# Kernel optimization log

Measured on AMD Instinct MI355X. Metric: run time of the kernel, lower is better.

## Reference

```python
import jax, jax.numpy as jnp
import numpy as np

B, M, N, D, NH, DH = 2, 2048, 2048, 1024, 16, 64
STD = 0.02

def setup_inputs() -> dict:
    key = jax.random.key(0)
    ks = jax.random.split(key, 7)
    query = jax.random.normal(ks[0], (B, M, D), dtype=jnp.float32)
    key_value = jax.random.normal(ks[1], (B, N, D), dtype=jnp.float32)
    key_padding_mask = jax.random.uniform(ks[2], (B, N)) < 0.1
    # torch Linear weight is (out,in); store as (in,out) for x @ W
    W_Q = STD * jax.random.truncated_normal(ks[3], -2.0, 2.0, (D, NH * DH), dtype=jnp.float32)
    W_K = STD * jax.random.truncated_normal(ks[4], -2.0, 2.0, (D, NH * DH), dtype=jnp.float32)
    W_V = STD * jax.random.truncated_normal(ks[5], -2.0, 2.0, (D, NH * DH), dtype=jnp.float32)
    W_O = STD * jax.random.truncated_normal(ks[6], -2.0, 2.0, (NH * DH, D), dtype=jnp.float32)
    return {"query": query, "key_value": key_value, "key_padding_mask": key_padding_mask,
            "W_Q": W_Q, "W_K": W_K, "W_V": W_V, "W_O": W_O}

def reference(query, key_value, key_padding_mask, W_Q, W_K, W_V, W_O):
    scale = 1.0 / jnp.sqrt(jnp.float32(DH))
    Q = (query @ W_Q).reshape(B, M, NH, DH)       # (B,M,H,dh)
    K = (key_value @ W_K).reshape(B, N, NH, DH)   # (B,N,H,dh)
    V = (key_value @ W_V).reshape(B, N, NH, DH)
    scores = jnp.einsum('bmhd,bnhd->bhmn', Q, K) * scale  # (B,H,M,N)
    scores = jnp.where(key_padding_mask[:, None, None, :], -jnp.inf, scores)
    attn = jax.nn.softmax(scores, axis=-1)
    out = jnp.einsum('bhmn,bnhd->bmhd', attn, V).reshape(B, M, NH * DH)
    return out @ W_O
```

## Files before the change

### kernel.cpp

```cpp
#include <hip/hip_runtime.h>
#include <math.h>

#define BB 2
#define SEQ 2048
#define DMODEL 1024
#define NHH 16
#define DHH 64

typedef __bf16 bf16;
typedef __attribute__((ext_vector_type(8))) __bf16 bf16x8;
typedef __attribute__((ext_vector_type(4))) float f32x4;
typedef __attribute__((ext_vector_type(16))) float f32x16;

#define C1f 0.18033688011112042f
#define C2f -5.770780163555854f

__device__ __forceinline__ uint32_t cvtpk_bf16(float lo, float hi) {
  uint32_t r;
  asm("v_cvt_pk_bf16_f32 %0, %1, %2" : "=v"(r) : "v"(lo), "v"(hi));
  return r;
}
__device__ __forceinline__ void pl32swap(uint32_t& a, uint32_t& b) {
  asm("v_permlane32_swap_b32 %0, %1" : "+v"(a), "+v"(b));
}

__device__ __forceinline__ void gl_lds16(const bf16* g, bf16* l) {
  __builtin_amdgcn_global_load_lds(
      (const __attribute__((address_space(1))) void*)g,
      (__attribute__((address_space(3))) void*)l, 16, 0, 0);
}

__global__ __launch_bounds__(256) void prep(const float* __restrict__ query,
                                            const float* __restrict__ key_value,
                                            bf16* __restrict__ qbf,
                                            bf16* __restrict__ kvbf,
                                            const float* __restrict__ W0, const float* __restrict__ W1,
                                            const float* __restrict__ W2, const float* __restrict__ W3,
                                            bf16* __restrict__ O0, bf16* __restrict__ O1,
                                            bf16* __restrict__ O2, bf16* __restrict__ O3) {
  __shared__ bf16 T[64][72];
  const int bid = blockIdx.x;
  const int t = threadIdx.x;
  if (bid >= 1024) {
    const int bidc = bid - 1024;
    const float* in = (bidc >> 11) ? key_value : query;
    bf16* out = (bidc >> 11) ? kvbf : qbf;
    const int i = (bidc & 2047) * 256 + t;
    const float4* p = (const float4*)in + 2 * (size_t)i;
    float4 a = p[0], b = p[1];
    bf16x8 v;
    v[0] = (bf16)a.x; v[1] = (bf16)a.y; v[2] = (bf16)a.z; v[3] = (bf16)a.w;
    v[4] = (bf16)b.x; v[5] = (bf16)b.y; v[6] = (bf16)b.z; v[7] = (bf16)b.w;
    *((bf16x8*)out + i) = v;
    return;
  }
  const float* W; bf16* O;
  switch (bid >> 8) {
    case 0: W = W0; O = O0; break;
    case 1: W = W1; O = O1; break;
    case 2: W = W2; O = O2; break;
    default: W = W3; O = O3; break;
  }
  const int n0 = (bid & 15) * 64, k0 = ((bid >> 4) & 15) * 64;
  {
    int k = t >> 2, ns = (t & 3) * 16;
    const float* g = W + (size_t)(k0 + k) * DMODEL + n0 + ns;
#pragma unroll
    for (int q = 0; q < 4; ++q) {
      float4 f = *(const float4*)(g + 4 * q);
      T[ns + 4 * q + 0][k] = (bf16)f.x;
      T[ns + 4 * q + 1][k] = (bf16)f.y;
      T[ns + 4 * q + 2][k] = (bf16)f.z;
      T[ns + 4 * q + 3][k] = (bf16)f.w;
    }
  }
  __syncthreads();
  {
    int n = t >> 2, ks = (t & 3) * 16;
    bf16x8 a = *(const bf16x8*)&T[n][ks];
    bf16x8 b = *(const bf16x8*)&T[n][ks + 8];
    bf16* o = O + (size_t)(n0 + n) * DMODEL + k0 + ks;
    *(bf16x8*)o = a;
    *(bf16x8*)(o + 8) = b;
  }
}

template <bool F32OUT>
__device__ __forceinline__ void gemm128_body(const bf16* __restrict__ A,
                                             const bf16* __restrict__ Bt,
                                             float* __restrict__ Cf,
                                             bf16* __restrict__ Cb,
                                             bf16* As0, bf16* Bs0,
                                             bf16* As1, bf16* Bs1) {
  const int t = threadIdx.x;
  const int lane = t & 63, wave = t >> 6;
  const int l15 = lane & 15, quad = lane >> 4;
  const int bm = blockIdx.y * 128, bn = blockIdx.x * 128;
  const int wr = wave >> 1, wc = wave & 1;

  const int srow = wave * 32 + (lane >> 3);
  const int sc = lane & 7;
  const int ca = sc ^ ((lane >> 3) & 7);
  const bf16* gA = A + (size_t)(bm + srow) * DMODEL + ca * 8;
  const bf16* gB = Bt + (size_t)(bn + srow) * DMODEL + ca * 8;
  const int lo = wave * 32 * 64;

  f32x4 acc[4][4] = {};

#define STAGE(KT, AS, BS)                                                \
  {                                                                      \
    const int kk = (KT) * 64;                                            \
    _Pragma("unroll") for (int j = 0; j < 4; ++j) {                      \
      gl_lds16(gA + (size_t)(j * 8) * DMODEL + kk, (AS) + lo + j * 512); \
      gl_lds16(gB + (size_t)(j * 8) * DMODEL + kk, (BS) + lo + j * 512); \
    }                                                                    \
  }

#define COMPUTE(AS, BS)                                                \
  {                                                                    \
    _Pragma("unroll") for (int ks = 0; ks < 2; ++ks) {                 \
      bf16x8 af[4], bfr[4];                                            \
      _Pragma("unroll") for (int mt = 0; mt < 4; ++mt) {               \
        int row = wr * 64 + mt * 16 + l15;                             \
        int s = (ks * 4 + quad) ^ (row & 7);                           \
        af[mt] = *(const bf16x8*)&(AS)[row * 64 + s * 8];              \
      }                                                                \
      _Pragma("unroll") for (int nt = 0; nt < 4; ++nt) {               \
        int row = wc * 64 + nt * 16 + l15;                             \
        int s = (ks * 4 + quad) ^ (row & 7);                           \
        bfr[nt] = *(const bf16x8*)&(BS)[row * 64 + s * 8];             \
      }                                                                \
      _Pragma("unroll") for (int mt = 0; mt < 4; ++mt)                 \
          _Pragma("unroll") for (int nt = 0; nt < 4; ++nt)             \
              acc[mt][nt] = __builtin_amdgcn_mfma_f32_16x16x32_bf16(   \
                  af[mt], bfr[nt], acc[mt][nt], 0, 0, 0);              \
    }                                                                  \
  }

  STAGE(0, As0, Bs0);
  __syncthreads();

  for (int kt = 0; kt < DMODEL / 64; kt += 2) {
    if (kt + 1 < DMODEL / 64) STAGE(kt + 1, As1, Bs1);
    COMPUTE(As0, Bs0);
    __syncthreads();
    if (kt + 2 < DMODEL / 64) STAGE(kt + 2, As0, Bs0);
    COMPUTE(As1, Bs1);
    __syncthreads();
  }
#undef STAGE
#undef COMPUTE

#pragma unroll
  for (int mt = 0; mt < 4; ++mt)
#pragma unroll
    for (int nt = 0; nt < 4; ++nt)
#pragma unroll
      for (int r = 0; r < 4; ++r) {
        int row = bm + wr * 64 + mt * 16 + quad * 4 + r;
        int col = bn + wc * 64 + nt * 16 + l15;
        if (F32OUT) Cf[(size_t)row * DMODEL + col] = acc[mt][nt][r];
        else Cb[(size_t)row * DMODEL + col] = (bf16)acc[mt][nt][r];
      }
}

__global__ __launch_bounds__(256, 2) void gemm_qkv(const bf16* __restrict__ qbf,
                                                   const bf16* __restrict__ kvbf,
                                                   const bf16* __restrict__ WtQ,
                                                   const bf16* __restrict__ WtK,
                                                   const bf16* __restrict__ WtV,
                                                   bf16* __restrict__ Qb,
                                                   bf16* __restrict__ Kb,
                                                   bf16* __restrict__ Vb) {
  __shared__ bf16 As0[128 * 64], Bs0[128 * 64];
  __shared__ bf16 As1[128 * 64], Bs1[128 * 64];
  const bf16 *A, *Bt; bf16* C;
  switch (blockIdx.z) {
    case 0: A = qbf; Bt = WtQ; C = Qb; break;
    case 1: A = kvbf; Bt = WtK; C = Kb; break;
    default: A = kvbf; Bt = WtV; C = Vb; break;
  }
  gemm128_body<false>(A, Bt, nullptr, C, As0, Bs0, As1, Bs1);
}

__global__ __launch_bounds__(256, 2) void gemm_out(const bf16* __restrict__ A,
                                                   const bf16* __restrict__ Wt,
                                                   float* __restrict__ C) {
  __shared__ bf16 As0[128 * 64], Bs0[128 * 64];
  __shared__ bf16 As1[128 * 64], Bs1[128 * 64];
  gemm128_body<true>(A, Wt, C, nullptr, As0, Bs0, As1, Bs1);
}

__global__ __launch_bounds__(256) void attn_mfma(const bf16* __restrict__ Qb,
                                                 const bf16* __restrict__ Kb,
                                                 const bf16* __restrict__ Vb,
                                                 const int* __restrict__ maskp,
                                                 bf16* __restrict__ Ob) {
  __shared__ bf16 Ks[2][64 * 64];
  __shared__ bf16 Vt[2][64][68];

  const int blk = blockIdx.x;
  const int h = blk & 15;
  const int b = (blk >> 4) & 1;
  const int qb = blk >> 5;
  const int t = threadIdx.x;
  const int wave = t >> 6, lane = t & 63;
  const int l31 = lane & 31, hi = lane >> 5;

  const int kr = t >> 2, kq = t & 3;
  const bf16* gK = Kb + (size_t)(b * SEQ + kr) * DMODEL + h * 64 + kq * 16;
  const int s0 = (kq * 2) ^ (kr & 7), s1 = (kq * 2 + 1) ^ (kr & 7);
  const int nv = (t & 31) * 2, dc = (t >> 5) * 8;
  const bf16* gV = Vb + (size_t)(b * SEQ + nv) * DMODEL + h * 64 + dc;
  const int* gM = maskp + b * SEQ;

  {
    bf16x8 k0 = *(const bf16x8*)(gK);
    bf16x8 k1 = *(const bf16x8*)(gK + 8);
    *(bf16x8*)&Ks[0][kr * 64 + s0 * 8] = k0;
    *(bf16x8*)&Ks[0][kr * 64 + s1 * 8] = k1;
    bf16x8 v0 = *(const bf16x8*)(gV);
    bf16x8 v1 = *(const bf16x8*)(gV + DMODEL);
    union U { bf16x8 v; uint32_t dw[4]; } a, c;
    a.v = v0; c.v = v1;
#pragma unroll
    for (int d2 = 0; d2 < 4; ++d2) {
      *(uint32_t*)&Vt[0][dc + 2 * d2 + 0][nv] = __builtin_amdgcn_perm(c.dw[d2], a.dw[d2], 0x05040100u);
      *(uint32_t*)&Vt[0][dc + 2 * d2 + 1][nv] = __builtin_amdgcn_perm(c.dw[d2], a.dw[d2], 0x07060302u);
    }
  }
  int mcur = gM[lane];

  bf16x8 qf[4];
#pragma unroll
  for (int ks = 0; ks < 4; ++ks) {
    const bf16* g = Qb + (size_t)(b * SEQ + qb * 128 + wave * 32 + l31) * DMODEL +
                    h * 64 + ks * 16 + hi * 8;
    qf[ks] = *(const bf16x8*)g;
  }

  f32x16 o0 = {}, o1 = {};
  float lsum = 0.f;

  __syncthreads();

  for (int it = 0; it < SEQ / 64; ++it) {
    const int p = it & 1;
    const bool more = (it + 1) < SEQ / 64;

    bf16x8 kreg0, kreg1, vreg0, vreg1;
    int mnext = 0;
    if (more) {
      const int nn = (it + 1) * 64;
      const bf16* gK2 = gK + (size_t)nn * DMODEL;
      const bf16* gV2 = gV + (size_t)nn * DMODEL;
      kreg0 = *(const bf16x8*)(gK2);
      kreg1 = *(const bf16x8*)(gK2 + 8);
      vreg0 = *(const bf16x8*)(gV2);
      vreg1 = *(const bf16x8*)(gV2 + DMODEL);
      mnext = gM[nn + lane];
    }

    f32x16 s0v = {}, s1v = {};
#pragma unroll
    for (int ks = 0; ks < 4; ++ks) {
      const int c = ks * 2 + hi;
      const int r0 = l31;
      const int r1 = 32 + l31;
      bf16x8 ka0 = *(const bf16x8*)&Ks[p][r0 * 64 + (c ^ (r0 & 7)) * 8];
      bf16x8 ka1 = *(const bf16x8*)&Ks[p][r1 * 64 + (c ^ (r1 & 7)) * 8];
      s0v = __builtin_amdgcn_mfma_f32_32x32x16_bf16(ka0, qf[ks], s0v, 0, 0, 0);
      s1v = __builtin_amdgcn_mfma_f32_32x32x16_bf16(ka1, qf[ks], s1v, 0, 0, 0);
    }

    const unsigned long long mb = __ballot(mcur == 0);

#pragma unroll
    for (int kt = 0; kt < 2; ++kt) {
      const f32x16 sv = kt ? s1v : s0v;
      const uint32_t ml = (uint32_t)(mb >> (kt * 32 + 4 * hi));
      float pm[16];
#pragma unroll
      for (int r = 0; r < 16; ++r) {
        const int bitc = (r & 3) + 8 * (r >> 2);
        float pex = __builtin_amdgcn_exp2f(sv[r] * C1f + C2f);
        pm[r] = ((ml >> bitc) & 1u) ? pex : 0.f;
        lsum += pm[r];
      }
      uint32_t w01 = cvtpk_bf16(pm[0], pm[1]),  w23 = cvtpk_bf16(pm[2], pm[3]);
      uint32_t w45 = cvtpk_bf16(pm[4], pm[5]),  w67 = cvtpk_bf16(pm[6], pm[7]);
      uint32_t w89 = cvtpk_bf16(pm[8], pm[9]),  wab = cvtpk_bf16(pm[10], pm[11]);
      uint32_t wcd = cvtpk_bf16(pm[12], pm[13]), wef = cvtpk_bf16(pm[14], pm[15]);
      pl32swap(w01, w45);
      pl32swap(w23, w67);
      pl32swap(w89, wcd);
      pl32swap(wab, wef);
      union BF { uint32_t u[4]; bf16x8 v; } f0, f1;
      f0.u[0] = w01; f0.u[1] = w23; f0.u[2] = w45; f0.u[3] = w67;
      f1.u[0] = w89; f1.u[1] = wab; f1.u[2] = wcd; f1.u[3] = wef;
      {
        bf16x8 va00 = *(const bf16x8*)&Vt[p][0 + l31][(kt * 2 + 0) * 16 + hi * 8];
        bf16x8 va01 = *(const bf16x8*)&Vt[p][0 + l31][(kt * 2 + 1) * 16 + hi * 8];
        o0 = __builtin_amdgcn_mfma_f32_32x32x16_bf16(va00, f0.v, o0, 0, 0, 0);
        o0 = __builtin_amdgcn_mfma_f32_32x32x16_bf16(va01, f1.v, o0, 0, 0, 0);
        bf16x8 va10 = *(const bf16x8*)&Vt[p][32 + l31][(kt * 2 + 0) * 16 + hi * 8];
        bf16x8 va11 = *(const bf16x8*)&Vt[p][32 + l31][(kt * 2 + 1) * 16 + hi * 8];
        o1 = __builtin_amdgcn_mfma_f32_32x32x16_bf16(va10, f0.v, o1, 0, 0, 0);
        o1 = __builtin_amdgcn_mfma_f32_32x32x16_bf16(va11, f1.v, o1, 0, 0, 0);
      }
    }

    if (more) {
      const int q = 1 - p;
      *(bf16x8*)&Ks[q][kr * 64 + s0 * 8] = kreg0;
      *(bf16x8*)&Ks[q][kr * 64 + s1 * 8] = kreg1;
      union U { bf16x8 v; uint32_t dw[4]; } a, c;
      a.v = vreg0; c.v = vreg1;
#pragma unroll
      for (int d2 = 0; d2 < 4; ++d2) {
        *(uint32_t*)&Vt[q][dc + 2 * d2 + 0][nv] = __builtin_amdgcn_perm(c.dw[d2], a.dw[d2], 0x05040100u);
        *(uint32_t*)&Vt[q][dc + 2 * d2 + 1][nv] = __builtin_amdgcn_perm(c.dw[d2], a.dw[d2], 0x07060302u);
      }
    }
    mcur = mnext;
    __syncthreads();
  }

  const float lt = lsum + __shfl_xor(lsum, 32);
  const float inv = 1.f / lt;
  bf16* gO = Ob + (size_t)(b * SEQ + qb * 128 + wave * 32 + l31) * DMODEL + h * 64;
#pragma unroll
  for (int g = 0; g < 4; ++g) {
    uint2 st0, st1;
    st0.x = cvtpk_bf16(o0[4 * g + 0] * inv, o0[4 * g + 1] * inv);
    st0.y = cvtpk_bf16(o0[4 * g + 2] * inv, o0[4 * g + 3] * inv);
    st1.x = cvtpk_bf16(o1[4 * g + 0] * inv, o1[4 * g + 1] * inv);
    st1.y = cvtpk_bf16(o1[4 * g + 2] * inv, o1[4 * g + 3] * inv);
    *(uint2*)(gO + 8 * g + 4 * hi) = st0;
    *(uint2*)(gO + 32 + 8 * g + 4 * hi) = st1;
  }
}

extern "C" void kernel_launch(void* const* d_in, const int* in_sizes, int n_in,
                              void* d_out, int out_size, void* d_ws, size_t ws_size,
                              hipStream_t stream) {
  (void)in_sizes; (void)n_in; (void)out_size; (void)ws_size;
  const float* query = (const float*)d_in[0];
  const float* key_value = (const float*)d_in[1];
  const int* mask = (const int*)d_in[2];
  const float* W_Q = (const float*)d_in[3];
  const float* W_K = (const float*)d_in[4];
  const float* W_V = (const float*)d_in[5];
  const float* W_O = (const float*)d_in[6];
  float* out = (float*)d_out;

  const size_t TOK = (size_t)BB * SEQ;
  const size_t TE = TOK * DMODEL;
  char* w = (char*)d_ws;
  bf16* qbf = (bf16*)w;   w += TE * 2;
  bf16* kvbf = (bf16*)w;  w += TE * 2;
  bf16* WtQ = (bf16*)w;   w += (size_t)DMODEL * DMODEL * 2;
  bf16* WtK = (bf16*)w;   w += (size_t)DMODEL * DMODEL * 2;
  bf16* WtV = (bf16*)w;   w += (size_t)DMODEL * DMODEL * 2;
  bf16* WtO = (bf16*)w;   w += (size_t)DMODEL * DMODEL * 2;
  bf16* Qbuf = (bf16*)w;  w += TE * 2;
  bf16* Kbuf = (bf16*)w;  w += TE * 2;
  bf16* Vbuf = (bf16*)w;  w += TE * 2;
  bf16* Obuf = (bf16*)w;  w += TE * 2;

  prep<<<5120, 256, 0, stream>>>(query, key_value, qbf, kvbf,
                                 W_Q, W_K, W_V, W_O, WtQ, WtK, WtV, WtO);

  gemm_qkv<<<dim3(DMODEL / 128, TOK / 128, 3), 256, 0, stream>>>(qbf, kvbf, WtQ, WtK, WtV,
                                                                 Qbuf, Kbuf, Vbuf);

  attn_mfma<<<BB * NHH * (SEQ / 128), 256, 0, stream>>>(Qbuf, Kbuf, Vbuf, mask, Obuf);

  gemm_out<<<dim3(DMODEL / 128, TOK / 128), 256, 0, stream>>>(Obuf, WtO, out);
}
```

Baseline: 212.5 us.

## Split key range across two wave groups per attention block and reduce partials

The attention block grows to 512 threads. Two groups of four waves each process half of the key/value sequence for the same 128 query rows, with separate double-buffered K/V shared tiles per group. At the end, the partial output accumulators and row sums are merged through shared memory reused from the K tile, and group 1 normalizes and writes the result. This doubles the resident waves per block to hide latency, at the cost of an extra LDS reduction. The K tile also drops its XOR swizzle in favour of padded rows, which may change bank-conflict behaviour.

```diff
diff --git a/kernel.cpp b/kernel.cpp
--- a/kernel.cpp
+++ b/kernel.cpp
@@ -191,13 +191,13 @@
   gemm128_body<true>(A, Wt, C, nullptr, As0, Bs0, As1, Bs1);
 }
 
-__global__ __launch_bounds__(256) void attn_mfma(const bf16* __restrict__ Qb,
-                                                 const bf16* __restrict__ Kb,
-                                                 const bf16* __restrict__ Vb,
-                                                 const int* __restrict__ maskp,
-                                                 bf16* __restrict__ Ob) {
-  __shared__ bf16 Ks[2][64 * 64];
-  __shared__ bf16 Vt[2][64][68];
+__global__ __launch_bounds__(512, 4) void attn_mfma(const bf16* __restrict__ Qb,
+                                                    const bf16* __restrict__ Kb,
+                                                    const bf16* __restrict__ Vb,
+                                                    const int* __restrict__ maskp,
+                                                    bf16* __restrict__ Ob) {
+  __shared__ bf16 Ks[2][2][64][68];
+  __shared__ bf16 Vt[2][2][64][68];
 
   const int blk = blockIdx.x;
   const int h = blk & 15;
@@ -205,28 +205,30 @@
   const int qb = blk >> 5;
   const int t = threadIdx.x;
   const int wave = t >> 6, lane = t & 63;
+  const int grp = wave >> 2;
+  const int w4 = wave & 3;
   const int l31 = lane & 31, hi = lane >> 5;
-
-  const int kr = t >> 2, kq = t & 3;
-  const bf16* gK = Kb + (size_t)(b * SEQ + kr) * DMODEL + h * 64 + kq * 16;
-  const int s0 = (kq * 2) ^ (kr & 7), s1 = (kq * 2 + 1) ^ (kr & 7);
-  const int nv = (t & 31) * 2, dc = (t >> 5) * 8;
-  const bf16* gV = Vb + (size_t)(b * SEQ + nv) * DMODEL + h * 64 + dc;
-  const int* gM = maskp + b * SEQ;
+  const int tl = t & 255;
+
+  const int kr = tl >> 2, kq = tl & 3;
+  const bf16* gK = Kb + (size_t)(b * SEQ + grp * 1024 + kr) * DMODEL + h * 64 + kq * 16;
+  const int nv = (tl & 31) * 2, dc = (tl >> 5) * 8;
+  const bf16* gV = Vb + (size_t)(b * SEQ + grp * 1024 + nv) * DMODEL + h * 64 + dc;
+  const int* gM = maskp + b * SEQ + grp * 1024;
 
   {
     bf16x8 k0 = *(const bf16x8*)(gK);
     bf16x8 k1 = *(const bf16x8*)(gK + 8);
-    *(bf16x8*)&Ks[0][kr * 64 + s0 * 8] = k0;
-    *(bf16x8*)&Ks[0][kr * 64 + s1 * 8] = k1;
+    *(bf16x8*)&Ks[grp][0][kr][kq * 16] = k0;
+    *(bf16x8*)&Ks[grp][0][kr][kq * 16 + 8] = k1;
     bf16x8 v0 = *(const bf16x8*)(gV);
     bf16x8 v1 = *(const bf16x8*)(gV + DMODEL);
     union U { bf16x8 v; uint32_t dw[4]; } a, c;
     a.v = v0; c.v = v1;
 #pragma unroll
     for (int d2 = 0; d2 < 4; ++d2) {
-      *(uint32_t*)&Vt[0][dc + 2 * d2 + 0][nv] = __builtin_amdgcn_perm(c.dw[d2], a.dw[d2], 0x05040100u);
-      *(uint32_t*)&Vt[0][dc + 2 * d2 + 1][nv] = __builtin_amdgcn_perm(c.dw[d2], a.dw[d2], 0x07060302u);
+      *(uint32_t*)&Vt[grp][0][dc + 2 * d2 + 0][nv] = __builtin_amdgcn_perm(c.dw[d2], a.dw[d2], 0x05040100u);
+      *(uint32_t*)&Vt[grp][0][dc + 2 * d2 + 1][nv] = __builtin_amdgcn_perm(c.dw[d2], a.dw[d2], 0x07060302u);
     }
   }
   int mcur = gM[lane];
@@ -234,7 +236,7 @@
   bf16x8 qf[4];
 #pragma unroll
   for (int ks = 0; ks < 4; ++ks) {
-    const bf16* g = Qb + (size_t)(b * SEQ + qb * 128 + wave * 32 + l31) * DMODEL +
+    const bf16* g = Qb + (size_t)(b * SEQ + qb * 128 + w4 * 32 + l31) * DMODEL +
                     h * 64 + ks * 16 + hi * 8;
     qf[ks] = *(const bf16x8*)g;
   }
@@ -244,9 +246,9 @@
 
   __syncthreads();
 
-  for (int it = 0; it < SEQ / 64; ++it) {
+  for (int it = 0; it < 16; ++it) {
     const int p = it & 1;
-    const bool more = (it + 1) < SEQ / 64;
+    const bool more = (it + 1) < 16;
 
     bf16x8 kreg0, kreg1, vreg0, vreg1;
     int mnext = 0;
@@ -264,11 +266,9 @@
     f32x16 s0v = {}, s1v = {};
 #pragma unroll
     for (int ks = 0; ks < 4; ++ks) {
-      const int c = ks * 2 + hi;
-      const int r0 = l31;
-      const int r1 = 32 + l31;
-      bf16x8 ka0 = *(const bf16x8*)&Ks[p][r0 * 64 + (c ^ (r0 & 7)) * 8];
-      bf16x8 ka1 = *(const bf16x8*)&Ks[p][r1 * 64 + (c ^ (r1 & 7)) * 8];
+      const int c = (ks * 2 + hi) * 8;
+      bf16x8 ka0 = *(const bf16x8*)&Ks[grp][p][l31][c];
+      bf16x8 ka1 = *(const bf16x8*)&Ks[grp][p][32 + l31][c];
       s0v = __builtin_amdgcn_mfma_f32_32x32x16_bf16(ka0, qf[ks], s0v, 0, 0, 0);
       s1v = __builtin_amdgcn_mfma_f32_32x32x16_bf16(ka1, qf[ks], s1v, 0, 0, 0);
     }
@@ -299,12 +299,12 @@
       f0.u[0] = w01; f0.u[1] = w23; f0.u[2] = w45; f0.u[3] = w67;
       f1.u[0] = w89; f1.u[1] = wab; f1.u[2] = wcd; f1.u[3] = wef;
       {
-        bf16x8 va00 = *(const bf16x8*)&Vt[p][0 + l31][(kt * 2 + 0) * 16 + hi * 8];
-        bf16x8 va01 = *(const bf16x8*)&Vt[p][0 + l31][(kt * 2 + 1) * 16 + hi * 8];
+        bf16x8 va00 = *(const bf16x8*)&Vt[grp][p][0 + l31][(kt * 2 + 0) * 16 + hi * 8];
+        bf16x8 va01 = *(const bf16x8*)&Vt[grp][p][0 + l31][(kt * 2 + 1) * 16 + hi * 8];
         o0 = __builtin_amdgcn_mfma_f32_32x32x16_bf16(va00, f0.v, o0, 0, 0, 0);
         o0 = __builtin_amdgcn_mfma_f32_32x32x16_bf16(va01, f1.v, o0, 0, 0, 0);
-        bf16x8 va10 = *(const bf16x8*)&Vt[p][32 + l31][(kt * 2 + 0) * 16 + hi * 8];
-        bf16x8 va11 = *(const bf16x8*)&Vt[p][32 + l31][(kt * 2 + 1) * 16 + hi * 8];
+        bf16x8 va10 = *(const bf16x8*)&Vt[grp][p][32 + l31][(kt * 2 + 0) * 16 + hi * 8];
+        bf16x8 va11 = *(const bf16x8*)&Vt[grp][p][32 + l31][(kt * 2 + 1) * 16 + hi * 8];
         o1 = __builtin_amdgcn_mfma_f32_32x32x16_bf16(va10, f0.v, o1, 0, 0, 0);
         o1 = __builtin_amdgcn_mfma_f32_32x32x16_bf16(va11, f1.v, o1, 0, 0, 0);
       }
@@ -312,32 +312,55 @@
 
     if (more) {
       const int q = 1 - p;
-      *(bf16x8*)&Ks[q][kr * 64 + s0 * 8] = kreg0;
-      *(bf16x8*)&Ks[q][kr * 64 + s1 * 8] = kreg1;
+      *(bf16x8*)&Ks[grp][q][kr][kq * 16] = kreg0;
+      *(bf16x8*)&Ks[grp][q][kr][kq * 16 + 8] = kreg1;
       union U { bf16x8 v; uint32_t dw[4]; } a, c;
       a.v = vreg0; c.v = vreg1;
 #pragma unroll
       for (int d2 = 0; d2 < 4; ++d2) {
-        *(uint32_t*)&Vt[q][dc + 2 * d2 + 0][nv] = __builtin_amdgcn_perm(c.dw[d2], a.dw[d2], 0x05040100u);
-        *(uint32_t*)&Vt[q][dc + 2 * d2 + 1][nv] = __builtin_amdgcn_perm(c.dw[d2], a.dw[d2], 0x07060302u);
+        *(uint32_t*)&Vt[grp][q][dc + 2 * d2 + 0][nv] = __builtin_amdgcn_perm(c.dw[d2], a.dw[d2], 0x05040100u);
+        *(uint32_t*)&Vt[grp][q][dc + 2 * d2 + 1][nv] = __builtin_amdgcn_perm(c.dw[d2], a.dw[d2], 0x07060302u);
       }
     }
     mcur = mnext;
     __syncthreads();
   }
 
-  const float lt = lsum + __shfl_xor(lsum, 32);
-  const float inv = 1.f / lt;
-  bf16* gO = Ob + (size_t)(b * SEQ + qb * 128 + wave * 32 + l31) * DMODEL + h * 64;
-#pragma unroll
-  for (int g = 0; g < 4; ++g) {
-    uint2 st0, st1;
-    st0.x = cvtpk_bf16(o0[4 * g + 0] * inv, o0[4 * g + 1] * inv);
-    st0.y = cvtpk_bf16(o0[4 * g + 2] * inv, o0[4 * g + 3] * inv);
-    st1.x = cvtpk_bf16(o1[4 * g + 0] * inv, o1[4 * g + 1] * inv);
-    st1.y = cvtpk_bf16(o1[4 * g + 2] * inv, o1[4 * g + 3] * inv);
-    *(uint2*)(gO + 8 * g + 4 * hi) = st0;
-    *(uint2*)(gO + 32 + 8 * g + 4 * hi) = st1;
+  const float ltp = lsum + __shfl_xor(lsum, 32);
+
+  float* sc = (float*)&Ks[0][0][0][0];
+  float* scO = sc + 256;
+
+  if (hi == 0) sc[wave * 32 + l31] = ltp;
+  if (grp == 0) {
+    float* dst = scO + ((size_t)(w4 * 64 + lane)) * 33;
+#pragma unroll
+    for (int r = 0; r < 16; ++r) {
+      dst[r] = o0[r];
+      dst[16 + r] = o1[r];
+    }
+  }
+  __syncthreads();
+  if (grp == 1) {
+    const float ltot = sc[w4 * 32 + l31] + sc[(4 + w4) * 32 + l31];
+    const float inv = 1.f / ltot;
+    const float* src = scO + ((size_t)(w4 * 64 + lane)) * 33;
+#pragma unroll
+    for (int r = 0; r < 16; ++r) {
+      o0[r] += src[r];
+      o1[r] += src[16 + r];
+    }
+    bf16* gO = Ob + (size_t)(b * SEQ + qb * 128 + w4 * 32 + l31) * DMODEL + h * 64;
+#pragma unroll
+    for (int g = 0; g < 4; ++g) {
+      uint2 st0, st1;
+      st0.x = cvtpk_bf16(o0[4 * g + 0] * inv, o0[4 * g + 1] * inv);
+      st0.y = cvtpk_bf16(o0[4 * g + 2] * inv, o0[4 * g + 3] * inv);
+      st1.x = cvtpk_bf16(o1[4 * g + 0] * inv, o1[4 * g + 1] * inv);
+      st1.y = cvtpk_bf16(o1[4 * g + 2] * inv, o1[4 * g + 3] * inv);
+      *(uint2*)(gO + 8 * g + 4 * hi) = st0;
+      *(uint2*)(gO + 32 + 8 * g + 4 * hi) = st1;
+    }
   }
 }
 
@@ -374,7 +397,7 @@
   gemm_qkv<<<dim3(DMODEL / 128, TOK / 128, 3), 256, 0, stream>>>(qbf, kvbf, WtQ, WtK, WtV,
                                                                  Qbuf, Kbuf, Vbuf);
 
-  attn_mfma<<<BB * NHH * (SEQ / 128), 256, 0, stream>>>(Qbuf, Kbuf, Vbuf, mask, Obuf);
+  attn_mfma<<<BB * NHH * (SEQ / 128), 512, 0, stream>>>(Qbuf, Kbuf, Vbuf, mask, Obuf);
 
   gemm_out<<<dim3(DMODEL / 128, TOK / 128), 256, 0, stream>>>(Obuf, WtO, out);
 }
```

Result: faster. 203.3 us (-4.3%).
